# Performance work log

Measured on AMD Instinct MI355X. Metric: run time of the kernel, lower is better.

## Reference

```python
import jax, jax.numpy as jnp
import numpy as np

KERNEL_SIZE = 5
KERNEL_NUM = 64
STRIDE = 1
PRIOR_VAR = 1.0


def setup_inputs() -> dict:
    key = jax.random.key(0)
    k1, k2 = jax.random.split(key)
    mu_in = jax.random.normal(k1, (128, 128, 128, 3), dtype=jnp.float32)
    # init: normal stddev 0.05 for w_mu, constant -4.6 for w_sigma
    w_mu = 0.05 * jax.random.normal(k2, (KERNEL_SIZE, KERNEL_SIZE, 3, KERNEL_NUM), dtype=jnp.float32)
    w_sigma = jnp.full((KERNEL_NUM,), -4.6, dtype=jnp.float32)
    return {"mu_in": mu_in, "w_mu": w_mu, "w_sigma": w_sigma}


def kl_regularizer_conv(mu, logvar):
    k = mu.shape[-1]
    mu2 = mu.reshape(-1, k)              # [k*k*C, kernel_num]
    n = mu2.shape[0]
    kl = -jnp.mean(1.0 + logvar
                   - jnp.log1p(jnp.exp(logvar)) / PRIOR_VAR
                   - jnp.sum(jnp.square(mu2), axis=0) / (n * PRIOR_VAR))
    kl = jnp.where(jnp.isnan(kl), jnp.float32(1e-05), kl)
    kl = jnp.where(jnp.isinf(kl), jnp.float32(1e-05), kl)
    return kl


def reference(mu_in, w_mu, w_sigma):
    B, H, W, C = mu_in.shape
    ks = KERNEL_SIZE
    kl_conv = kl_regularizer_conv(w_mu, w_sigma)
    w_sigma_2 = jnp.log1p(jnp.exp(w_sigma))  # softplus

    dn = ('NHWC', 'HWIO', 'NHWC')
    mu_out = jax.lax.conv_general_dilated(
        mu_in, w_mu, window_strides=(STRIDE, STRIDE), padding='VALID',
        dimension_numbers=dn)  # [B, Ho, Wo, kernel_num]

    # Per-patch sum of squares == sum-pool conv over squared input summed over C
    # (mathematically identical to extract_patches -> square -> sum, no im2col blowup)
    sq = jnp.sum(jnp.square(mu_in), axis=-1, keepdims=True)  # [B,H,W,1]
    ones_k = jnp.ones((ks, ks, 1, 1), dtype=mu_in.dtype)
    patch_ss = jax.lax.conv_general_dilated(
        sq, ones_k, window_strides=(STRIDE, STRIDE), padding='VALID',
        dimension_numbers=dn)  # [B, Ho, Wo, 1]
    x_dim = jnp.float32(ks * ks * C)
    # broadcast: softplus(w_sigma)[kn] * (sum_sq / x_dim)[B,Ho,Wo,1]
    Sigma_out = w_sigma_2 * (patch_ss / x_dim)  # [B, Ho, Wo, kernel_num]

    Ho = mu_out.shape[1]
    Sigma_out = Sigma_out.reshape(B, Ho, Ho, KERNEL_NUM)
    return (mu_out, Sigma_out, kl_conv)
```

## Files before the change

### kernel.cpp

```cpp
#include <hip/hip_runtime.h>
#include <hip/hip_bf16.h>
#include <math.h>

#define KN 64
#define HO 124
#define KP 104
#define NOUT (128LL * 124 * 124 * 64)
#define NG 31

typedef short bfrag8 __attribute__((ext_vector_type(8)));
typedef float ffrag4 __attribute__((ext_vector_type(4)));

__device__ __forceinline__ unsigned short f2bf(float f) {
    union { float f; unsigned u; } x;
    x.f = f;
    unsigned r = x.u + 0x7fffu + ((x.u >> 16) & 1u);
    return (unsigned short)(r >> 16);
}
__device__ __forceinline__ unsigned pack2(float a, float b) {
    return (unsigned)f2bf(a) | ((unsigned)f2bf(b) << 16);
}

__device__ __forceinline__ int im_off(int row, int wo, int half) {
    return (((row * 128 + wo) * 32) + half * 16) ^ (((wo >> 2) & 7) << 4);
}

__global__ void prep_kernel(const float* __restrict__ w_mu,
                            const float* __restrict__ w_sigma,
                            unsigned short* __restrict__ w_bf,
                            float* __restrict__ sp_out) {
    const int tid = threadIdx.x;
    const int n = tid >> 2;
    const int kbase = (tid & 3) * 26;
#pragma unroll
    for (int kk = 0; kk < 26; ++kk) {
        const int k = kbase + kk;
        float v = 0.f;
        if (k < 80) {
            const int r = k >> 4, t = k & 15;
            if (t < 15) v = w_mu[(r * 15 + t) * KN + n];
        }
        w_bf[n * KP + k] = f2bf(v);
    }
    if (tid < KN) sp_out[tid] = log1pf(expf(w_sigma[tid]));
}

__global__ void kl_kernel(const float* __restrict__ w_mu,
                          const float* __restrict__ w_sigma,
                          float* __restrict__ out_kl) {
    int kn = threadIdx.x;
    float s = 0.f;
#pragma unroll
    for (int i = 0; i < 75; ++i) {
        float m = w_mu[i * KN + kn];
        s = fmaf(m, m, s);
    }
    float lv = w_sigma[kn];
    float sp = log1pf(expf(lv));
    float val = 1.0f + lv - sp - s * (1.0f / 75.0f);
#pragma unroll
    for (int off = 32; off > 0; off >>= 1) val += __shfl_down(val, off);
    if (kn == 0) {
        float kl = -(val / 64.0f);
        if (isnan(kl) || isinf(kl)) kl = 1e-5f;
        out_kl[0] = kl;
    }
}

template <int OFF>
__device__ __forceinline__ void im_fill(const float* __restrict__ mu_in,
                                        unsigned short* s_im, int b, int ho0,
                                        int lane, int wo) {
#pragma unroll
    for (int j = 0; j < 4; ++j) {
        const int row = ((lane >> 5) << 2) + j;
        uint4* dst0 =
            reinterpret_cast<uint4*>((char*)s_im + im_off(row, wo, 0));
        uint4* dst1 =
            reinterpret_cast<uint4*>((char*)s_im + im_off(row, wo, 1));
        if (wo >= 124) {
            *dst0 = make_uint4(0u, 0u, 0u, 0u);
            *dst1 = make_uint4(0u, 0u, 0u, 0u);
            continue;
        }
        const float* p =
            mu_in + ((size_t)(b * 128 + ho0 + row) * 384 + wo * 3 - OFF);
        float w[20];
        float4 f;
        f = reinterpret_cast<const float4*>(p)[0];
        w[0] = f.x; w[1] = f.y; w[2] = f.z; w[3] = f.w;
        f = reinterpret_cast<const float4*>(p)[1];
        w[4] = f.x; w[5] = f.y; w[6] = f.z; w[7] = f.w;
        f = reinterpret_cast<const float4*>(p)[2];
        w[8] = f.x; w[9] = f.y; w[10] = f.z; w[11] = f.w;
        f = reinterpret_cast<const float4*>(p)[3];
        w[12] = f.x; w[13] = f.y; w[14] = f.z; w[15] = f.w;
        if (OFF >= 2) {
            f = reinterpret_cast<const float4*>(p)[4];
            w[16] = f.x; w[17] = f.y; w[18] = f.z; w[19] = f.w;
        } else {
            w[16] = 0.f; w[17] = 0.f; w[18] = 0.f; w[19] = 0.f;
        }
        unsigned u0 = pack2(w[OFF + 0], w[OFF + 1]);
        unsigned u1 = pack2(w[OFF + 2], w[OFF + 3]);
        unsigned u2 = pack2(w[OFF + 4], w[OFF + 5]);
        unsigned u3 = pack2(w[OFF + 6], w[OFF + 7]);
        unsigned u4 = pack2(w[OFF + 8], w[OFF + 9]);
        unsigned u5 = pack2(w[OFF + 10], w[OFF + 11]);
        unsigned u6 = pack2(w[OFF + 12], w[OFF + 13]);
        unsigned u7 = pack2(w[OFF + 14], 0.0f);
        *dst0 = make_uint4(u0, u1, u2, u3);
        *dst1 = make_uint4(u4, u5, u6, u7);
    }
}

__global__ __launch_bounds__(256, 4) void conv_kernel(
    const float* __restrict__ mu_in,
    const unsigned short* __restrict__ w_bf,
    const float* __restrict__ sp_in,
    float* __restrict__ mu_out,
    float* __restrict__ sig_out) {

    __shared__ __align__(16) unsigned short s_im[8 * 128 * 16];
    __shared__ __align__(16) float s_cs[8 * 128];
    __shared__ float s_ssn[4 * 128];
    __shared__ float s_sp[KN];

    const int bid = blockIdx.x;
    const int b = bid / NG;
    const int ho0 = (bid % NG) * 4;
    const int tid = threadIdx.x;
    const int lane = tid & 63;
    const int wid = tid >> 6;
    const int llo = lane & 15;
    const int lhi = lane >> 4;

    bfrag8 afr[4][3];
#pragma unroll
    for (int mt = 0; mt < 4; ++mt)
#pragma unroll
        for (int ks = 0; ks < 3; ++ks)
            afr[mt][ks] = *reinterpret_cast<const bfrag8*>(
                &w_bf[(mt * 16 + llo) * KP + ks * 32 + lhi * 8]);
    if (tid < KN) s_sp[tid] = sp_in[tid];

    {
        const int r = tid >> 5;
        const int c4 = (tid & 31) << 2;
        const float* p = mu_in + ((size_t)(b * 128 + ho0 + r) * 384 + c4 * 3);
        float4 f0 = reinterpret_cast<const float4*>(p)[0];
        float4 f1 = reinterpret_cast<const float4*>(p)[1];
        float4 f2 = reinterpret_cast<const float4*>(p)[2];
        float4 cs;
        cs.x = f0.x * f0.x + f0.y * f0.y + f0.z * f0.z;
        cs.y = f0.w * f0.w + f1.x * f1.x + f1.y * f1.y;
        cs.z = f1.z * f1.z + f1.w * f1.w + f2.x * f2.x;
        cs.w = f2.y * f2.y + f2.z * f2.z + f2.w * f2.w;
        *reinterpret_cast<float4*>(&s_cs[r * 128 + c4]) = cs;
    }

    {
        const int wo = wid + ((lane & 31) << 2);
        switch (wid) {
            case 0: im_fill<0>(mu_in, s_im, b, ho0, lane, wo); break;
            case 1: im_fill<3>(mu_in, s_im, b, ho0, lane, wo); break;
            case 2: im_fill<2>(mu_in, s_im, b, ho0, lane, wo); break;
            default: im_fill<1>(mu_in, s_im, b, ho0, lane, wo); break;
        }
    }
    __syncthreads();

    for (int i = tid; i < 512; i += 256) {
        const int hl = i >> 7, wo = i & 127;
        float v = 0.f;
        if (wo < HO) {
            float s = 0.f;
#pragma unroll
            for (int r = 0; r < 5; ++r)
#pragma unroll
                for (int d = 0; d < 5; ++d) s += s_cs[(hl + r) * 128 + wo + d];
            v = s * (1.0f / 75.0f);
        }
        s_ssn[hl * 128 + wo] = v;
    }
    __syncthreads();

    ffrag4 acc[2][4];
#pragma unroll
    for (int hl = 0; hl < 4; ++hl) {
#pragma unroll
        for (int nt = 0; nt < 2; ++nt)
#pragma unroll
            for (int mt = 0; mt < 4; ++mt)
                acc[nt][mt] = (ffrag4){0.f, 0.f, 0.f, 0.f};

#pragma unroll
        for (int nt = 0; nt < 2; ++nt) {
            const int wo = (wid * 2 + nt) * 16 + llo;
#pragma unroll
            for (int ks = 0; ks < 3; ++ks) {
                const int k0 = ks * 32 + lhi * 8;
                const int r = k0 >> 4;
                bfrag8 bfr = (bfrag8){0, 0, 0, 0, 0, 0, 0, 0};
                if (r < 5) {
                    bfr = *reinterpret_cast<const bfrag8*>(
                        (char*)s_im + im_off(hl + r, wo, (k0 & 15) >> 3));
                }
#pragma unroll
                for (int mt = 0; mt < 4; ++mt)
                    acc[nt][mt] = __builtin_amdgcn_mfma_f32_16x16x32_bf16(
                        afr[mt][ks], bfr, acc[nt][mt], 0, 0, 0);
            }
        }

        const size_t orow = (size_t)(b * HO + ho0 + hl) * (size_t)(HO * KN);
#pragma unroll
        for (int nt = 0; nt < 2; ++nt) {
            const int wo = (wid * 2 + nt) * 16 + llo;
            if (wo < HO) {
                const float ssn = s_ssn[hl * 128 + wo];
                const size_t obase = orow + (size_t)wo * KN;
#pragma unroll
                for (int mt = 0; mt < 4; ++mt) {
                    const int knb = mt * 16 + lhi * 4;
                    const float4 sp4 =
                        *reinterpret_cast<const float4*>(&s_sp[knb]);
                    *reinterpret_cast<float4*>(&mu_out[obase + knb]) =
                        make_float4(acc[nt][mt][0], acc[nt][mt][1],
                                    acc[nt][mt][2], acc[nt][mt][3]);
                    *reinterpret_cast<float4*>(&sig_out[obase + knb]) =
                        make_float4(sp4.x * ssn, sp4.y * ssn, sp4.z * ssn,
                                    sp4.w * ssn);
                }
            }
        }
    }
}

extern "C" void kernel_launch(void* const* d_in, const int* in_sizes, int n_in,
                              void* d_out, int out_size, void* d_ws,
                              size_t ws_size, hipStream_t stream) {
    const float* mu_in = (const float*)d_in[0];
    const float* w_mu = (const float*)d_in[1];
    const float* w_sigma = (const float*)d_in[2];
    float* out = (float*)d_out;

    float* mu_out = out;
    float* sig_out = out + NOUT;
    float* kl_out = out + 2 * NOUT;

    unsigned short* w_bf = (unsigned short*)d_ws;
    float* sp_ws = (float*)((char*)d_ws + KN * KP * 2);

    prep_kernel<<<1, 256, 0, stream>>>(w_mu, w_sigma, w_bf, sp_ws);
    conv_kernel<<<128 * NG, 256, 0, stream>>>(mu_in, w_bf, sp_ws, mu_out,
                                              sig_out);
    kl_kernel<<<1, 64, 0, stream>>>(w_mu, w_sigma, kl_out);
}
```

Before: 242.4 us.

## Precompute bf16 row-window buffer in a separate kernel before the conv

```diff
diff --git a/kernel.cpp b/kernel.cpp
--- a/kernel.cpp
+++ b/kernel.cpp
@@ -11,6 +11,12 @@
 typedef short bfrag8 __attribute__((ext_vector_type(8)));
 typedef float ffrag4 __attribute__((ext_vector_type(4)));
 
+#define WS_X_OFF 0
+#define WS_CS_OFF 67108864ULL
+#define WS_WBF_OFF (WS_CS_OFF + 8388608ULL)
+#define WS_SP_OFF (WS_WBF_OFF + 13312ULL)
+#define WS_NEED (WS_SP_OFF + 256ULL)
+
 __device__ __forceinline__ unsigned short f2bf(float f) {
     union { float f; unsigned u; } x;
     x.f = f;
@@ -19,10 +25,6 @@
 }
 __device__ __forceinline__ unsigned pack2(float a, float b) {
     return (unsigned)f2bf(a) | ((unsigned)f2bf(b) << 16);
-}
-
-__device__ __forceinline__ int im_off(int row, int wo, int half) {
-    return (((row * 128 + wo) * 32) + half * 16) ^ (((wo >> 2) & 7) << 4);
 }
 
 __global__ void prep_kernel(const float* __restrict__ w_mu,
@@ -65,6 +67,152 @@
         if (isnan(kl) || isinf(kl)) kl = 1e-5f;
         out_kl[0] = kl;
     }
+}
+
+__global__ void x_build_kernel(const float* __restrict__ mu_in,
+                               uint4* __restrict__ X4,
+                               float* __restrict__ cs_ws) {
+    __shared__ __align__(16) float s_row[384];
+    const int bh = blockIdx.x;
+    const int tid = threadIdx.x;
+    const float* src = mu_in + (size_t)bh * 384;
+    if (tid < 96)
+        reinterpret_cast<float4*>(s_row)[tid] =
+            reinterpret_cast<const float4*>(src)[tid];
+    __syncthreads();
+    if (tid < 128) {
+        float a = s_row[3 * tid], b2 = s_row[3 * tid + 1],
+              c2 = s_row[3 * tid + 2];
+        cs_ws[(size_t)bh * 128 + tid] = a * a + b2 * b2 + c2 * c2;
+    }
+    const int wo = tid >> 1, half = tid & 1;
+    unsigned u[4];
+#pragma unroll
+    for (int p = 0; p < 4; ++p) {
+        const int t0 = half * 8 + 2 * p, t1 = t0 + 1;
+        float v0 = 0.f, v1 = 0.f;
+        if (wo < 124) {
+            v0 = (t0 < 15) ? s_row[wo * 3 + t0] : 0.f;
+            v1 = (t1 < 15) ? s_row[wo * 3 + t1] : 0.f;
+        }
+        u[p] = pack2(v0, v1);
+    }
+    const int c = wo * 2 + (half ^ ((wo >> 2) & 1));
+    X4[(size_t)bh * 256 + c] = make_uint4(u[0], u[1], u[2], u[3]);
+}
+
+__global__ __launch_bounds__(256, 4) void conv2_kernel(
+    const uint4* __restrict__ X4, const float* __restrict__ cs_ws,
+    const unsigned short* __restrict__ w_bf, const float* __restrict__ sp_in,
+    float* __restrict__ mu_out, float* __restrict__ sig_out) {
+
+    __shared__ __align__(16) unsigned short s_im[8 * 128 * 16];
+    __shared__ __align__(16) float s_cs[8 * 128];
+    __shared__ float s_ssn[4 * 128];
+    __shared__ float s_sp[KN];
+
+    const int bid = blockIdx.x;
+    const int b = bid / NG;
+    const int h0 = (bid % NG) * 4;
+    const int tid = threadIdx.x;
+    const int lane = tid & 63;
+    const int wid = tid >> 6;
+    const int llo = lane & 15;
+    const int lhi = lane >> 4;
+
+    {
+        const uint4* xs = X4 + (size_t)(b * 128 + h0) * 256;
+        uint4* d = reinterpret_cast<uint4*>(s_im);
+#pragma unroll
+        for (int i = 0; i < 8; ++i) d[tid + i * 256] = xs[tid + i * 256];
+        reinterpret_cast<uint4*>(s_cs)[tid] = reinterpret_cast<const uint4*>(
+            cs_ws + (size_t)(b * 128 + h0) * 128)[tid];
+    }
+    bfrag8 afr[4][3];
+#pragma unroll
+    for (int mt = 0; mt < 4; ++mt)
+#pragma unroll
+        for (int ks = 0; ks < 3; ++ks)
+            afr[mt][ks] = *reinterpret_cast<const bfrag8*>(
+                &w_bf[(mt * 16 + llo) * KP + ks * 32 + lhi * 8]);
+    if (tid < KN) s_sp[tid] = sp_in[tid];
+    __syncthreads();
+
+#pragma unroll
+    for (int it = 0; it < 2; ++it) {
+        const int idx = tid + it * 256;
+        const int hl = idx >> 7, wo = idx & 127;
+        float v = 0.f;
+        if (wo < HO) {
+            float s = 0.f;
+#pragma unroll
+            for (int r = 0; r < 5; ++r) {
+                const float* cr = &s_cs[(hl + r) * 128 + wo];
+                s += cr[0] + cr[1] + cr[2] + cr[3] + cr[4];
+            }
+            v = s * (1.0f / 75.0f);
+        }
+        s_ssn[idx] = v;
+    }
+    __syncthreads();
+
+    float4 sp4[4];
+#pragma unroll
+    for (int mt = 0; mt < 4; ++mt)
+        sp4[mt] = *reinterpret_cast<const float4*>(&s_sp[mt * 16 + lhi * 4]);
+
+    const uint4* sim4 = reinterpret_cast<const uint4*>(s_im);
+#pragma unroll
+    for (int hl = 0; hl < 4; ++hl) {
+        ffrag4 acc[2][4];
+#pragma unroll
+        for (int nt = 0; nt < 2; ++nt)
+#pragma unroll
+            for (int mt = 0; mt < 4; ++mt)
+                acc[nt][mt] = (ffrag4){0.f, 0.f, 0.f, 0.f};
+
+#pragma unroll
+        for (int nt = 0; nt < 2; ++nt) {
+            const int wo = (wid * 2 + nt) * 16 + llo;
+            const int swz = (lhi & 1) ^ ((wo >> 2) & 1);
+#pragma unroll
+            for (int ks = 0; ks < 3; ++ks) {
+                const int rk = 2 * ks + (lhi >> 1);
+                bfrag8 bfr = (bfrag8){0, 0, 0, 0, 0, 0, 0, 0};
+                if (rk < 5)
+                    bfr = *reinterpret_cast<const bfrag8*>(
+                        &sim4[(hl + rk) * 256 + wo * 2 + swz]);
+#pragma unroll
+                for (int mt = 0; mt < 4; ++mt)
+                    acc[nt][mt] = __builtin_amdgcn_mfma_f32_16x16x32_bf16(
+                        afr[mt][ks], bfr, acc[nt][mt], 0, 0, 0);
+            }
+        }
+
+        const size_t orow = (size_t)(b * HO + h0 + hl) * (size_t)(HO * KN);
+#pragma unroll
+        for (int nt = 0; nt < 2; ++nt) {
+            const int wo = (wid * 2 + nt) * 16 + llo;
+            if (wo < HO) {
+                const float ssn = s_ssn[hl * 128 + wo];
+                float* mp = mu_out + orow + (size_t)wo * KN;
+                float* gp = sig_out + orow + (size_t)wo * KN;
+#pragma unroll
+                for (int mt = 0; mt < 4; ++mt) {
+                    const int knb = mt * 16 + lhi * 4;
+                    ffrag4 sv = {sp4[mt].x * ssn, sp4[mt].y * ssn,
+                                 sp4[mt].z * ssn, sp4[mt].w * ssn};
+                    __builtin_nontemporal_store(acc[nt][mt],
+                                                (ffrag4*)(mp + knb));
+                    __builtin_nontemporal_store(sv, (ffrag4*)(gp + knb));
+                }
+            }
+        }
+    }
+}
+
+__device__ __forceinline__ int im_off(int row, int wo, int half) {
+    return (((row * 128 + wo) * 32) + half * 16) ^ (((wo >> 2) & 7) << 4);
 }
 
 template <int OFF>
@@ -158,7 +306,6 @@
         cs.w = f2.y * f2.y + f2.z * f2.z + f2.w * f2.w;
         *reinterpret_cast<float4*>(&s_cs[r * 128 + c4]) = cs;
     }
-
     {
         const int wo = wid + ((lane & 31) << 2);
         switch (wid) {
@@ -249,11 +396,22 @@
     float* sig_out = out + NOUT;
     float* kl_out = out + 2 * NOUT;
 
-    unsigned short* w_bf = (unsigned short*)d_ws;
-    float* sp_ws = (float*)((char*)d_ws + KN * KP * 2);
+    const bool big = ws_size >= WS_NEED;
+    char* ws = (char*)d_ws;
+    unsigned short* w_bf =
+        (unsigned short*)(big ? ws + WS_WBF_OFF : ws);
+    float* sp_ws = (float*)((big ? ws + WS_WBF_OFF : ws) + KN * KP * 2);
 
     prep_kernel<<<1, 256, 0, stream>>>(w_mu, w_sigma, w_bf, sp_ws);
-    conv_kernel<<<128 * NG, 256, 0, stream>>>(mu_in, w_bf, sp_ws, mu_out,
-                                              sig_out);
+    if (big) {
+        uint4* X4 = (uint4*)(ws + WS_X_OFF);
+        float* cs_ws = (float*)(ws + WS_CS_OFF);
+        x_build_kernel<<<128 * 128, 256, 0, stream>>>(mu_in, X4, cs_ws);
+        conv2_kernel<<<128 * NG, 256, 0, stream>>>(X4, cs_ws, w_bf, sp_ws,
+                                                   mu_out, sig_out);
+    } else {
+        conv_kernel<<<128 * NG, 256, 0, stream>>>(mu_in, w_bf, sp_ws, mu_out,
+                                                  sig_out);
+    }
     kl_kernel<<<1, 64, 0, stream>>>(w_mu, w_sigma, kl_out);
 }
```

New measurement: 359.6 us. 1.48x slower.

## Split fused conv kernel into separate ssn, mu-conv and sigma-broadcast kernels

Applied to the files above, without the earlier changes.

```diff
diff --git a/kernel.cpp b/kernel.cpp
--- a/kernel.cpp
+++ b/kernel.cpp
@@ -7,6 +7,10 @@
 #define KP 104
 #define NOUT (128LL * 124 * 124 * 64)
 #define NG 31
+
+#define WS_SSN_OFF 0ULL
+#define WS_WBF_OFF 7872512ULL
+#define WS_SP_OFF 7885824ULL
 
 typedef short bfrag8 __attribute__((ext_vector_type(8)));
 typedef float ffrag4 __attribute__((ext_vector_type(4)));
@@ -64,6 +68,74 @@
         float kl = -(val / 64.0f);
         if (isnan(kl) || isinf(kl)) kl = 1e-5f;
         out_kl[0] = kl;
+    }
+}
+
+__global__ void ssn_kernel(const float* __restrict__ mu_in,
+                           float* __restrict__ ssn_ws) {
+    __shared__ __align__(16) float s_cs[8 * 128];
+    const int bid = blockIdx.x;
+    const int b = bid / NG;
+    const int ho0 = (bid % NG) * 4;
+    const int tid = threadIdx.x;
+
+    {
+        const int r = tid >> 5;
+        const int c4 = (tid & 31) << 2;
+        const float* p = mu_in + ((size_t)(b * 128 + ho0 + r) * 384 + c4 * 3);
+        float4 f0 = reinterpret_cast<const float4*>(p)[0];
+        float4 f1 = reinterpret_cast<const float4*>(p)[1];
+        float4 f2 = reinterpret_cast<const float4*>(p)[2];
+        float4 cs;
+        cs.x = f0.x * f0.x + f0.y * f0.y + f0.z * f0.z;
+        cs.y = f0.w * f0.w + f1.x * f1.x + f1.y * f1.y;
+        cs.z = f1.z * f1.z + f1.w * f1.w + f2.x * f2.x;
+        cs.w = f2.y * f2.y + f2.z * f2.z + f2.w * f2.w;
+        *reinterpret_cast<float4*>(&s_cs[r * 128 + c4]) = cs;
+    }
+    __syncthreads();
+
+#pragma unroll
+    for (int it = 0; it < 2; ++it) {
+        const int idx = tid + it * 256;
+        const int hl = idx >> 7, wo = idx & 127;
+        if (wo < HO) {
+            float s = 0.f;
+#pragma unroll
+            for (int r = 0; r < 5; ++r) {
+                const float* cr = &s_cs[(hl + r) * 128 + wo];
+                s += cr[0] + cr[1] + cr[2] + cr[3] + cr[4];
+            }
+            ssn_ws[((size_t)(b * HO) + ho0 + hl) * HO + wo] = s * (1.0f / 75.0f);
+        }
+    }
+}
+
+__global__ __launch_bounds__(256) void sigma_kernel(
+    const float* __restrict__ ssn_ws, const float* __restrict__ sp_in,
+    float4* __restrict__ sig_out) {
+    const long long TOT = 128LL * 124 * 124 * 16;
+    const long long NT = (long long)gridDim.x * 256;
+    const long long g0 = (long long)blockIdx.x * 256 + threadIdx.x;
+    const float4 sp4 = reinterpret_cast<const float4*>(sp_in)[g0 & 15];
+
+    long long g = g0;
+    for (; g + 3 * NT < TOT; g += 4 * NT) {
+        const float s0 = ssn_ws[g >> 4];
+        const float s1 = ssn_ws[(g + NT) >> 4];
+        const float s2 = ssn_ws[(g + 2 * NT) >> 4];
+        const float s3 = ssn_ws[(g + 3 * NT) >> 4];
+        sig_out[g] = make_float4(sp4.x * s0, sp4.y * s0, sp4.z * s0, sp4.w * s0);
+        sig_out[g + NT] =
+            make_float4(sp4.x * s1, sp4.y * s1, sp4.z * s1, sp4.w * s1);
+        sig_out[g + 2 * NT] =
+            make_float4(sp4.x * s2, sp4.y * s2, sp4.z * s2, sp4.w * s2);
+        sig_out[g + 3 * NT] =
+            make_float4(sp4.x * s3, sp4.y * s3, sp4.z * s3, sp4.w * s3);
+    }
+    for (; g < TOT; g += NT) {
+        const float s = ssn_ws[g >> 4];
+        sig_out[g] = make_float4(sp4.x * s, sp4.y * s, sp4.z * s, sp4.w * s);
     }
 }
 
@@ -114,17 +186,12 @@
     }
 }
 
-__global__ __launch_bounds__(256, 4) void conv_kernel(
+__global__ __launch_bounds__(256, 4) void conv_mu_kernel(
     const float* __restrict__ mu_in,
     const unsigned short* __restrict__ w_bf,
-    const float* __restrict__ sp_in,
-    float* __restrict__ mu_out,
-    float* __restrict__ sig_out) {
+    float* __restrict__ mu_out) {
 
     __shared__ __align__(16) unsigned short s_im[8 * 128 * 16];
-    __shared__ __align__(16) float s_cs[8 * 128];
-    __shared__ float s_ssn[4 * 128];
-    __shared__ float s_sp[KN];
 
     const int bid = blockIdx.x;
     const int b = bid / NG;
@@ -142,22 +209,6 @@
         for (int ks = 0; ks < 3; ++ks)
             afr[mt][ks] = *reinterpret_cast<const bfrag8*>(
                 &w_bf[(mt * 16 + llo) * KP + ks * 32 + lhi * 8]);
-    if (tid < KN) s_sp[tid] = sp_in[tid];
-
-    {
-        const int r = tid >> 5;
-        const int c4 = (tid & 31) << 2;
-        const float* p = mu_in + ((size_t)(b * 128 + ho0 + r) * 384 + c4 * 3);
-        float4 f0 = reinterpret_cast<const float4*>(p)[0];
-        float4 f1 = reinterpret_cast<const float4*>(p)[1];
-        float4 f2 = reinterpret_cast<const float4*>(p)[2];
-        float4 cs;
-        cs.x = f0.x * f0.x + f0.y * f0.y + f0.z * f0.z;
-        cs.y = f0.w * f0.w + f1.x * f1.x + f1.y * f1.y;
-        cs.z = f1.z * f1.z + f1.w * f1.w + f2.x * f2.x;
-        cs.w = f2.y * f2.y + f2.z * f2.z + f2.w * f2.w;
-        *reinterpret_cast<float4*>(&s_cs[r * 128 + c4]) = cs;
-    }
 
     {
         const int wo = wid + ((lane & 31) << 2);
@@ -170,24 +221,9 @@
     }
     __syncthreads();
 
-    for (int i = tid; i < 512; i += 256) {
-        const int hl = i >> 7, wo = i & 127;
-        float v = 0.f;
-        if (wo < HO) {
-            float s = 0.f;
-#pragma unroll
-            for (int r = 0; r < 5; ++r)
-#pragma unroll
-                for (int d = 0; d < 5; ++d) s += s_cs[(hl + r) * 128 + wo + d];
-            v = s * (1.0f / 75.0f);
-        }
-        s_ssn[hl * 128 + wo] = v;
-    }
-    __syncthreads();
-
-    ffrag4 acc[2][4];
 #pragma unroll
     for (int hl = 0; hl < 4; ++hl) {
+        ffrag4 acc[2][4];
 #pragma unroll
         for (int nt = 0; nt < 2; ++nt)
 #pragma unroll
@@ -218,19 +254,13 @@
         for (int nt = 0; nt < 2; ++nt) {
             const int wo = (wid * 2 + nt) * 16 + llo;
             if (wo < HO) {
-                const float ssn = s_ssn[hl * 128 + wo];
                 const size_t obase = orow + (size_t)wo * KN;
 #pragma unroll
                 for (int mt = 0; mt < 4; ++mt) {
                     const int knb = mt * 16 + lhi * 4;
-                    const float4 sp4 =
-                        *reinterpret_cast<const float4*>(&s_sp[knb]);
                     *reinterpret_cast<float4*>(&mu_out[obase + knb]) =
                         make_float4(acc[nt][mt][0], acc[nt][mt][1],
                                     acc[nt][mt][2], acc[nt][mt][3]);
-                    *reinterpret_cast<float4*>(&sig_out[obase + knb]) =
-                        make_float4(sp4.x * ssn, sp4.y * ssn, sp4.z * ssn,
-                                    sp4.w * ssn);
                 }
             }
         }
@@ -249,11 +279,15 @@
     float* sig_out = out + NOUT;
     float* kl_out = out + 2 * NOUT;
 
-    unsigned short* w_bf = (unsigned short*)d_ws;
-    float* sp_ws = (float*)((char*)d_ws + KN * KP * 2);
+    char* ws = (char*)d_ws;
+    float* ssn_ws = (float*)(ws + WS_SSN_OFF);
+    unsigned short* w_bf = (unsigned short*)(ws + WS_WBF_OFF);
+    float* sp_ws = (float*)(ws + WS_SP_OFF);
 
     prep_kernel<<<1, 256, 0, stream>>>(w_mu, w_sigma, w_bf, sp_ws);
-    conv_kernel<<<128 * NG, 256, 0, stream>>>(mu_in, w_bf, sp_ws, mu_out,
-                                              sig_out);
+    ssn_kernel<<<128 * NG, 256, 0, stream>>>(mu_in, ssn_ws);
+    conv_mu_kernel<<<128 * NG, 256, 0, stream>>>(mu_in, w_bf, mu_out);
+    sigma_kernel<<<2048, 256, 0, stream>>>(ssn_ws, sp_ws,
+                                           (float4*)sig_out);
     kl_kernel<<<1, 64, 0, stream>>>(w_mu, w_sigma, kl_out);
 }
```

Result: faster. 228.5 us (-5.7%).
